# Kernel tuning notes

Hardware: AMD Instinct MI355X
Metric: run time of the kernel (lower is better)

Reference implementation:

```python
import jax, jax.numpy as jnp
import numpy as np

HIDDEN = 2048
NUM_HEADS = 16
NUM_KV_HEADS = 4
HEAD_DIM = HIDDEN // NUM_HEADS            # 128
Q_PER_KV = NUM_HEADS // NUM_KV_HEADS      # 4
GROUP_SIZE = (Q_PER_KV + 2) * HEAD_DIM    # 768
TOTAL_PROJ = NUM_KV_HEADS * GROUP_SIZE    # 3072
SEQ, BATCH = 2048, 2


def setup_inputs() -> dict:
    key = jax.random.key(0)
    k1, k2, k3 = jax.random.split(key, 3)
    x = jax.random.normal(k1, (SEQ, BATCH, HIDDEN), dtype=jnp.float32)
    weight_qkv = jax.random.normal(k2, (TOTAL_PROJ, HIDDEN), dtype=jnp.float32) * 0.02
    weight_proj = jax.random.normal(k3, (HIDDEN, NUM_HEADS * HEAD_DIM), dtype=jnp.float32) * 0.02
    return {"x": x, "weight_qkv": weight_qkv, "weight_proj": weight_proj}


def reference(x, weight_qkv, weight_proj):
    seq, batch, hidden = x.shape
    q_size = Q_PER_KV * HEAD_DIM

    # fused grouped QKV projection: [S*B, TOTAL_PROJ]
    qkv = x.reshape(-1, hidden) @ weight_qkv.T
    qkv = qkv.reshape(-1, NUM_KV_HEADS, GROUP_SIZE)
    q = qkv[:, :, :q_size].reshape(seq, batch, NUM_HEADS, HEAD_DIM)
    k = qkv[:, :, q_size:q_size + HEAD_DIM].reshape(seq, batch, NUM_KV_HEADS, HEAD_DIM)
    v = qkv[:, :, q_size + HEAD_DIM:].reshape(seq, batch, NUM_KV_HEADS, HEAD_DIM)

    # GQA: repeat_interleave kv heads to match q heads
    k = jnp.repeat(k, Q_PER_KV, axis=2)
    v = jnp.repeat(v, Q_PER_KV, axis=2)

    # [b, h, s, d]
    q = q.transpose(1, 2, 0, 3)
    k = k.transpose(1, 2, 0, 3)
    v = v.transpose(1, 2, 0, 3)

    scale = 1.0 / np.sqrt(HEAD_DIM)
    scores = jnp.einsum('bhqd,bhkd->bhqk', q, k) * scale
    causal = jnp.tril(jnp.ones((seq, seq), dtype=bool))
    scores = jnp.where(causal, scores, jnp.float32(-jnp.inf))
    probs = jax.nn.softmax(scores, axis=-1)
    attn = jnp.einsum('bhqk,bhkd->bhqd', probs, v)

    # back to [s, b, h*d] then output projection
    attn = attn.transpose(2, 0, 1, 3).reshape(seq * batch, NUM_HEADS * HEAD_DIM)
    out = attn @ weight_proj.T
    return out.reshape(seq, batch, hidden)
```

## Files before the change

### kernel.cpp

```cpp
#include <hip/hip_runtime.h>

#define SEQ 2048
#define BATCH 2
#define HIDDEN 2048
#define NHEADS 16
#define NKV 4
#define HD 128
#define GROUP 768
#define TPROJ 3072
#define NTOK (SEQ*BATCH)

typedef __attribute__((ext_vector_type(8))) __bf16 bf16x8;
typedef __attribute__((ext_vector_type(8))) unsigned short ushort8_t;
typedef __attribute__((ext_vector_type(4))) float f32x4;

union U8cast { ushort8_t u; bf16x8 b; };
__device__ inline bf16x8 as_bf(ushort8_t u) { U8cast c; c.u = u; return c.b; }

union Bf16U { __bf16 h; unsigned short u; };

__device__ inline unsigned short f2bf(float f) {
    unsigned int u = __float_as_uint(f);
    return (unsigned short)((u + 0x7FFFu + ((u >> 16) & 1u)) >> 16);
}

__device__ inline ushort8_t load8_f32_bf16(const float* __restrict__ p) {
    float4 v0 = *(const float4*)p;
    float4 v1 = *(const float4*)(p + 4);
    ushort8_t u;
    u[0] = f2bf(v0.x); u[1] = f2bf(v0.y); u[2] = f2bf(v0.z); u[3] = f2bf(v0.w);
    u[4] = f2bf(v1.x); u[5] = f2bf(v1.y); u[6] = f2bf(v1.z); u[7] = f2bf(v1.w);
    return u;
}

__device__ inline float exp2a(float x) {
    float r; asm("v_exp_f32 %0, %1" : "=v"(r) : "v"(x)); return r;
}

__device__ inline void gload_lds16(const unsigned short* g, unsigned short* l) {
    __builtin_amdgcn_global_load_lds(
        (const __attribute__((address_space(1))) void*)g,
        (__attribute__((address_space(3))) void*)l, 16, 0, 0);
}

#define CONV_N0 ((size_t)NTOK * HIDDEN)
#define CONV_N1 ((size_t)TPROJ * HIDDEN)
#define CONV_N2 ((size_t)HIDDEN * HIDDEN)
__global__ __launch_bounds__(256) void conv3_kernel(
    const float* __restrict__ x, const float* __restrict__ wq, const float* __restrict__ wp,
    unsigned short* __restrict__ xb, unsigned short* __restrict__ wqb, unsigned short* __restrict__ wpb)
{
    size_t i = (size_t)(blockIdx.x * 256 + threadIdx.x) * 8;
    if (i < CONV_N0) {
        *(ushort8_t*)(xb + i) = load8_f32_bf16(x + i);
    } else if (i < CONV_N0 + CONV_N1) {
        size_t j = i - CONV_N0;
        *(ushort8_t*)(wqb + j) = load8_f32_bf16(wq + j);
    } else {
        size_t j = i - CONV_N0 - CONV_N1;
        *(ushort8_t*)(wpb + j) = load8_f32_bf16(wp + j);
    }
}

template<bool OUT_BF16>
__global__ __launch_bounds__(512, 2) void gemm256_kernel(
    const unsigned short* __restrict__ A, const unsigned short* __restrict__ B,
    void* __restrict__ Cv, int M, int N, int K)
{
    __shared__ unsigned short lds[2][2][256 * 64];

    const int t = threadIdx.x, lane = t & 63, w = t >> 6;
    const int wm = w >> 2, wn = w & 3;
    const int l16 = lane & 15, lg = lane >> 4;

    const int cpx = (int)gridDim.x >> 3;
    const int wg  = ((int)blockIdx.x & 7) * cpx + ((int)blockIdx.x >> 3);
    const int nbn = N >> 8;
    const int m0 = (wg / nbn) << 8, n0 = (wg % nbn) << 8;
    const int NKT = K >> 6;

    const int srow = lane >> 3;
    const int scol = ((lane & 7) ^ srow) << 3;

    f32x4 acc[8][4] = {};

    auto stage = [&](const unsigned short* __restrict__ G, int g0, int kt, int op) {
        const int k0 = kt << 6;
        unsigned short* Ld = lds[kt & 1][op];
#pragma unroll
        for (int i = 0; i < 4; ++i) {
            const int r = w * 32 + i * 8;
            gload_lds16(G + (size_t)(g0 + r + srow) * K + k0 + scol, Ld + r * 64);
        }
    };

    stage(A, m0, 0, 0); stage(B, n0, 0, 1);
    stage(A, m0, 1, 0); stage(B, n0, 1, 1);

    for (int kt = 0; kt < NKT; ++kt) {
        const unsigned short* As_ = lds[kt & 1][0];
        const unsigned short* Bs_ = lds[kt & 1][1];

        if (kt < NKT - 1) asm volatile("s_waitcnt vmcnt(8)" ::: "memory");
        else              asm volatile("s_waitcnt vmcnt(0)" ::: "memory");
        __builtin_amdgcn_sched_barrier(0);
        __builtin_amdgcn_s_barrier();
        __builtin_amdgcn_sched_barrier(0);

        bf16x8 aR[8], b0R[4], b1R[4];

#pragma unroll
        for (int i = 0; i < 4; ++i)
#pragma unroll
            for (int s = 0; s < 2; ++s) {
                int row  = wm * 128 + i * 16 + l16;
                int slot = ((s << 2) | lg) ^ (l16 & 7);
                aR[i * 2 + s] = as_bf(*(const ushort8_t*)&As_[row * 64 + slot * 8]);
            }
#pragma unroll
        for (int j = 0; j < 2; ++j)
#pragma unroll
            for (int s = 0; s < 2; ++s) {
                int row  = wn * 64 + j * 16 + l16;
                int slot = ((s << 2) | lg) ^ (l16 & 7);
                b0R[j * 2 + s] = as_bf(*(const ushort8_t*)&Bs_[row * 64 + slot * 8]);
            }
        __builtin_amdgcn_s_setprio(1);
#pragma unroll
        for (int i = 0; i < 4; ++i)
#pragma unroll
            for (int j = 0; j < 2; ++j)
#pragma unroll
                for (int s = 0; s < 2; ++s)
                    acc[i][j] = __builtin_amdgcn_mfma_f32_16x16x32_bf16(aR[i*2+s], b0R[j*2+s], acc[i][j], 0, 0, 0);
        __builtin_amdgcn_s_setprio(0);

#pragma unroll
        for (int j = 0; j < 2; ++j)
#pragma unroll
            for (int s = 0; s < 2; ++s) {
                int row  = wn * 64 + 32 + j * 16 + l16;
                int slot = ((s << 2) | lg) ^ (l16 & 7);
                b1R[j * 2 + s] = as_bf(*(const ushort8_t*)&Bs_[row * 64 + slot * 8]);
            }
        __builtin_amdgcn_s_setprio(1);
#pragma unroll
        for (int i = 0; i < 4; ++i)
#pragma unroll
            for (int j = 0; j < 2; ++j)
#pragma unroll
                for (int s = 0; s < 2; ++s)
                    acc[i][2 + j] = __builtin_amdgcn_mfma_f32_16x16x32_bf16(aR[i*2+s], b1R[j*2+s], acc[i][2 + j], 0, 0, 0);
        __builtin_amdgcn_s_setprio(0);

        __builtin_amdgcn_sched_barrier(0);
        __builtin_amdgcn_s_barrier();
        __builtin_amdgcn_sched_barrier(0);
        if (kt + 2 < NKT) stage(B, n0, kt + 2, 1);
        __builtin_amdgcn_sched_barrier(0);

#pragma unroll
        for (int i = 0; i < 4; ++i)
#pragma unroll
            for (int s = 0; s < 2; ++s) {
                int row  = wm * 128 + 64 + i * 16 + l16;
                int slot = ((s << 2) | lg) ^ (l16 & 7);
                aR[i * 2 + s] = as_bf(*(const ushort8_t*)&As_[row * 64 + slot * 8]);
            }
        __builtin_amdgcn_s_setprio(1);
#pragma unroll
        for (int i = 0; i < 4; ++i)
#pragma unroll
            for (int j = 0; j < 2; ++j)
#pragma unroll
                for (int s = 0; s < 2; ++s)
                    acc[4 + i][2 + j] = __builtin_amdgcn_mfma_f32_16x16x32_bf16(aR[i*2+s], b1R[j*2+s], acc[4 + i][2 + j], 0, 0, 0);
        __builtin_amdgcn_s_setprio(0);

        __builtin_amdgcn_sched_barrier(0);
        __builtin_amdgcn_s_barrier();
        __builtin_amdgcn_sched_barrier(0);
        if (kt + 2 < NKT) stage(A, m0, kt + 2, 0);
        __builtin_amdgcn_sched_barrier(0);

        __builtin_amdgcn_s_setprio(1);
#pragma unroll
        for (int i = 0; i < 4; ++i)
#pragma unroll
            for (int j = 0; j < 2; ++j)
#pragma unroll
                for (int s = 0; s < 2; ++s)
                    acc[4 + i][j] = __builtin_amdgcn_mfma_f32_16x16x32_bf16(aR[i*2+s], b0R[j*2+s], acc[4 + i][j], 0, 0, 0);
        __builtin_amdgcn_s_setprio(0);
    }

#pragma unroll
    for (int ia = 0; ia < 8; ++ia)
#pragma unroll
        for (int jb = 0; jb < 4; ++jb)
#pragma unroll
            for (int r = 0; r < 4; ++r) {
                int row = m0 + wm * 128 + (ia >> 2) * 64 + (ia & 3) * 16 + lg * 4 + r;
                int col = n0 + wn * 64 + (jb >> 1) * 32 + (jb & 1) * 16 + l16;
                if (OUT_BF16)
                    ((unsigned short*)Cv)[(size_t)row * N + col] = f2bf(acc[ia][jb][r]);
                else
                    ((float*)Cv)[(size_t)row * N + col] = acc[ia][jb][r];
            }
}

__global__ __launch_bounds__(512, 2) void gemm_tall_kernel(
    const unsigned short* __restrict__ A, const unsigned short* __restrict__ B,
    float* __restrict__ C, int M, int N, int K)
{
    __shared__ unsigned short ldsA[2][256 * 64];
    __shared__ unsigned short ldsB[2][128 * 64];

    const int t = threadIdx.x, lane = t & 63, w = t >> 6;
    const int wm = w >> 1, wn = w & 1;
    const int l16 = lane & 15, lg = lane >> 4;

    const int cpx = (int)gridDim.x >> 3;
    const int wg  = ((int)blockIdx.x & 7) * cpx + ((int)blockIdx.x >> 3);
    const int nbn = N >> 7;
    const int m0 = (wg / nbn) << 8, n0 = (wg % nbn) << 7;
    const int NKT = K >> 6;

    const int srow = lane >> 3;
    const int scol = ((lane & 7) ^ srow) << 3;

    f32x4 acc[4][4] = {};

    auto stageA = [&](int kt) {
        const int k0 = kt << 6;
        unsigned short* Ld = ldsA[kt & 1];
#pragma unroll
        for (int i = 0; i < 4; ++i) {
            const int r = w * 32 + i * 8;
            gload_lds16(A + (size_t)(m0 + r + srow) * K + k0 + scol, Ld + r * 64);
        }
    };
    auto stageB = [&](int kt) {
        const int k0 = kt << 6;
        unsigned short* Ld = ldsB[kt & 1];
#pragma unroll
        for (int i = 0; i < 2; ++i) {
            const int r = w * 16 + i * 8;
            gload_lds16(B + (size_t)(n0 + r + srow) * K + k0 + scol, Ld + r * 64);
        }
    };

    stageA(0); stageB(0);
    stageA(1); stageB(1);

    for (int kt = 0; kt < NKT; ++kt) {
        const unsigned short* As_ = ldsA[kt & 1];
        const unsigned short* Bs_ = ldsB[kt & 1];

        if (kt < NKT - 1) asm volatile("s_waitcnt vmcnt(6)" ::: "memory");
        else              asm volatile("s_waitcnt vmcnt(0)" ::: "memory");
        __builtin_amdgcn_sched_barrier(0);
        __builtin_amdgcn_s_barrier();
        __builtin_amdgcn_sched_barrier(0);

        bf16x8 aR[4], b0R[4], b1R[4];

#pragma unroll
        for (int i = 0; i < 2; ++i)
#pragma unroll
            for (int s = 0; s < 2; ++s) {
                int row  = wm * 64 + i * 16 + l16;
                int slot = ((s << 2) | lg) ^ (l16 & 7);
                aR[i * 2 + s] = as_bf(*(const ushort8_t*)&As_[row * 64 + slot * 8]);
            }
#pragma unroll
        for (int j = 0; j < 2; ++j)
#pragma unroll
            for (int s = 0; s < 2; ++s) {
                int row  = wn * 64 + j * 16 + l16;
                int slot = ((s << 2) | lg) ^ (l16 & 7);
                b0R[j * 2 + s] = as_bf(*(const ushort8_t*)&Bs_[row * 64 + slot * 8]);
            }
        __builtin_amdgcn_s_setprio(1);
#pragma unroll
        for (int i = 0; i < 2; ++i)
#pragma unroll
            for (int j = 0; j < 2; ++j)
#pragma unroll
                for (int s = 0; s < 2; ++s)
                    acc[i][j] = __builtin_amdgcn_mfma_f32_16x16x32_bf16(aR[i*2+s], b0R[j*2+s], acc[i][j], 0, 0, 0);
        __builtin_amdgcn_s_setprio(0);

#pragma unroll
        for (int j = 0; j < 2; ++j)
#pragma unroll
            for (int s = 0; s < 2; ++s) {
                int row  = wn * 64 + 32 + j * 16 + l16;
                int slot = ((s << 2) | lg) ^ (l16 & 7);
                b1R[j * 2 + s] = as_bf(*(const ushort8_t*)&Bs_[row * 64 + slot * 8]);
            }
        __builtin_amdgcn_s_setprio(1);
#pragma unroll
        for (int i = 0; i < 2; ++i)
#pragma unroll
            for (int j = 0; j < 2; ++j)
#pragma unroll
                for (int s = 0; s < 2; ++s)
                    acc[i][2 + j] = __builtin_amdgcn_mfma_f32_16x16x32_bf16(aR[i*2+s], b1R[j*2+s], acc[i][2 + j], 0, 0, 0);
        __builtin_amdgcn_s_setprio(0);

        __builtin_amdgcn_sched_barrier(0);
        __builtin_amdgcn_s_barrier();
        __builtin_amdgcn_sched_barrier(0);
        if (kt + 2 < NKT) stageB(kt + 2);
        __builtin_amdgcn_sched_barrier(0);

#pragma unroll
        for (int i = 0; i < 2; ++i)
#pragma unroll
            for (int s = 0; s < 2; ++s) {
                int row  = wm * 64 + 32 + i * 16 + l16;
                int slot = ((s << 2) | lg) ^ (l16 & 7);
                aR[i * 2 + s] = as_bf(*(const ushort8_t*)&As_[row * 64 + slot * 8]);
            }
        __builtin_amdgcn_s_setprio(1);
#pragma unroll
        for (int i = 0; i < 2; ++i)
#pragma unroll
            for (int j = 0; j < 2; ++j)
#pragma unroll
                for (int s = 0; s < 2; ++s)
                    acc[2 + i][2 + j] = __builtin_amdgcn_mfma_f32_16x16x32_bf16(aR[i*2+s], b1R[j*2+s], acc[2 + i][2 + j], 0, 0, 0);
        __builtin_amdgcn_s_setprio(0);

        __builtin_amdgcn_sched_barrier(0);
        __builtin_amdgcn_s_barrier();
        __builtin_amdgcn_sched_barrier(0);
        if (kt + 2 < NKT) stageA(kt + 2);
        __builtin_amdgcn_sched_barrier(0);

        __builtin_amdgcn_s_setprio(1);
#pragma unroll
        for (int i = 0; i < 2; ++i)
#pragma unroll
            for (int j = 0; j < 2; ++j)
#pragma unroll
                for (int s = 0; s < 2; ++s)
                    acc[2 + i][j] = __builtin_amdgcn_mfma_f32_16x16x32_bf16(aR[i*2+s], b0R[j*2+s], acc[2 + i][j], 0, 0, 0);
        __builtin_amdgcn_s_setprio(0);
    }

#pragma unroll
    for (int i = 0; i < 4; ++i)
#pragma unroll
        for (int j = 0; j < 4; ++j)
#pragma unroll
            for (int r = 0; r < 4; ++r) {
                int row = m0 + wm * 64 + i * 16 + lg * 4 + r;
                int col = n0 + wn * 64 + j * 16 + l16;
                C[(size_t)row * N + col] = acc[i][j][r];
            }
}

__global__ __launch_bounds__(256) void vtrans_kernel(const unsigned short* __restrict__ qkv,
                                                     unsigned short* __restrict__ vT)
{
    const int t = threadIdx.x;
    const int s0 = blockIdx.x * 128 + (t & 15) * 8;
    const int bk = blockIdx.y;
    const int b_idx = bk >> 2;
    const int voff = (bk & 3) * GROUP + 640;
    const int d0 = (t >> 4) * 8;
    ushort8_t in[8];
#pragma unroll
    for (int j = 0; j < 8; ++j)
        in[j] = *(const ushort8_t*)(qkv + (size_t)((s0 + j) * BATCH + b_idx) * TPROJ + voff + d0);
#pragma unroll
    for (int dd = 0; dd < 8; ++dd) {
        ushort8_t ov;
#pragma unroll
        for (int j = 0; j < 8; ++j) ov[j] = in[j][dd];
        *(ushort8_t*)(vT + (size_t)(bk * HD + d0 + dd) * SEQ + s0) = ov;
    }
}

__global__ __launch_bounds__(256, 4) void attn_kernel(const unsigned short* __restrict__ qkv,
                                                      const unsigned short* __restrict__ vT,
                                                      unsigned short* __restrict__ attn_out)
{
    __shared__ unsigned short Ks[64][128];
    __shared__ unsigned short Vt[2][128][64];

    const int t = threadIdx.x, lane = t & 63, w = t >> 6;
    const int l16 = lane & 15, lg = lane >> 4;

    const int bid = (int)blockIdx.x;
    const int qt  = 127 - (bid >> 3);
    const int bk  = bid & 7;
    const int b_idx = bk >> 2;
    const int kvh   = bk & 3;
    const int qb0   = qt * 16;
    const int qoff  = kvh * GROUP + w * HD;
    const int koff  = kvh * GROUP + 512;
    const int vrow0 = (b_idx * NKV + kvh) * HD;
    const int h     = kvh * 4 + w;

    const float SCL2 = 0.08838834764831845f * 1.44269504f;
    const float THRU = 8.0f / SCL2;

    ushort8_t qf[4];
    {
        size_t qrow = (size_t)((qb0 + l16) * BATCH + b_idx) * TPROJ + qoff;
#pragma unroll
        for (int kc = 0; kc < 4; ++kc)
            qf[kc] = *(const ushort8_t*)(qkv + qrow + kc * 32 + lg * 8);
    }

    f32x4 o[8] = {};
    float mstate = -1e30f, lstate = 0.f, negm2 = 0.f;

    const int nIter = (qt >> 2) + 1;

    auto stageK = [&](int it) {
        const int kv0 = it << 6;
#pragma unroll
        for (int i = 0; i < 4; ++i) {
            int rl = w * 16 + i * 4 + (lane >> 4);
            int pr = 32 * ((rl >> 4) & 1) + 8 * ((rl >> 2) & 3) + 4 * (rl >> 5) + (rl & 3);
            int g  = (lane & 15) ^ (rl & 7);
            gload_lds16(qkv + (size_t)((kv0 + pr) * BATCH + b_idx) * TPROJ + koff + g * 8,
                        &Ks[w * 16 + i * 4][0]);
        }
    };
    auto stageV = [&](int it) {
        const int kv0 = it << 6;
        const int buf = it & 1;
#pragma unroll
        for (int i = 0; i < 4; ++i) {
            int rl = w * 32 + i * 8 + (lane >> 3);
            int g  = (lane & 7) ^ ((lane >> 3) & 7);
            gload_lds16(vT + (size_t)(vrow0 + rl) * SEQ + kv0 + g * 8,
                        &Vt[buf][w * 32 + i * 8][0]);
        }
    };

    stageK(0); stageV(0);

    for (int it = 0; it < nIter; ++it) {
        const int kv0 = it * 64;
        const int vbuf = it & 1;

        asm volatile("s_waitcnt vmcnt(0)" ::: "memory");
        __builtin_amdgcn_sched_barrier(0);
        __builtin_amdgcn_s_barrier();
        __builtin_amdgcn_sched_barrier(0);

        if (it + 1 < nIter) stageV(it + 1);
        __builtin_amdgcn_sched_barrier(0);

        f32x4 s[4] = {};
        __builtin_amdgcn_s_setprio(1);
#pragma unroll
        for (int nf = 0; nf < 4; ++nf)
#pragma unroll
            for (int kc = 0; kc < 4; ++kc) {
                int phys = (kc * 4 + lg) ^ (l16 & 7);
                ushort8_t kb = *(const ushort8_t*)&Ks[nf * 16 + l16][phys * 8];
                s[nf] = __builtin_amdgcn_mfma_f32_16x16x32_bf16(as_bf(kb), as_bf(qf[kc]), s[nf], 0, 0, 0);
            }
        __builtin_amdgcn_s_setprio(0);

        __builtin_amdgcn_sched_barrier(0);
        __builtin_amdgcn_s_barrier();
        __builtin_amdgcn_sched_barrier(0);
        if (it + 1 < nIter) stageK(it + 1);
        __builtin_amdgcn_sched_barrier(0);

        if (it == nIter - 1) {
            const int q_g = qb0 + l16;
#pragma unroll
            for (int nf = 0; nf < 4; ++nf)
#pragma unroll
                for (int r = 0; r < 4; ++r) {
                    int kv_g = kv0 + 32 * (nf & 1) + 8 * lg + 4 * (nf >> 1) + r;
                    if (kv_g > q_g) s[nf][r] = -1e30f;
                }
        }

        float a0 = fmaxf(fmaxf(s[0][0], s[0][1]), fmaxf(s[0][2], s[0][3]));
        float a1 = fmaxf(fmaxf(s[1][0], s[1][1]), fmaxf(s[1][2], s[1][3]));
        float a2 = fmaxf(fmaxf(s[2][0], s[2][1]), fmaxf(s[2][2], s[2][3]));
        float a3 = fmaxf(fmaxf(s[3][0], s[3][1]), fmaxf(s[3][2], s[3][3]));
        float rmax = fmaxf(fmaxf(a0, a1), fmaxf(a2, a3));
        rmax = fmaxf(rmax, __shfl_xor(rmax, 16));
        rmax = fmaxf(rmax, __shfl_xor(rmax, 32));

        if (!__all(rmax - mstate <= THRU)) {
            float mn = fmaxf(mstate, rmax);
            float corr = exp2a((mstate - mn) * SCL2);
            mstate = mn;
            negm2  = -mn * SCL2;
            lstate *= corr;
            float co[4];
#pragma unroll
            for (int r = 0; r < 4; ++r) co[r] = __shfl(corr, 4 * lg + r);
#pragma unroll
            for (int f = 0; f < 8; ++f)
#pragma unroll
                for (int r = 0; r < 4; ++r) o[f][r] *= co[r];
        }

        float rs0 = 0.f, rs1 = 0.f;
#pragma unroll
        for (int nf = 0; nf < 4; ++nf)
#pragma unroll
            for (int r = 0; r < 4; ++r) {
                float pv = exp2a(fmaf(s[nf][r], SCL2, negm2));
                s[nf][r] = pv;
                if (nf < 2) rs0 += pv; else rs1 += pv;
            }
        float rsum = rs0 + rs1;
        rsum += __shfl_xor(rsum, 16);
        rsum += __shfl_xor(rsum, 32);
        lstate += rsum;

        ushort8_t paf[2];
#pragma unroll
        for (int c = 0; c < 2; ++c)
#pragma unroll
            for (int e = 0; e < 8; ++e) {
                Bf16U cv; cv.h = (__bf16)((e < 4) ? s[c][e] : s[2 + c][e - 4]);
                paf[c][e] = cv.u;
            }

        __builtin_amdgcn_s_setprio(1);
#pragma unroll
        for (int c = 0; c < 2; ++c)
#pragma unroll
            for (int f = 0; f < 8; ++f) {
                int phys = (c * 4 + lg) ^ (l16 & 7);
                ushort8_t vf = *(const ushort8_t*)&Vt[vbuf][l16 + 16 * f][phys * 8];
                o[f] = __builtin_amdgcn_mfma_f32_16x16x32_bf16(as_bf(paf[c]), as_bf(vf), o[f], 0, 0, 0);
            }
        __builtin_amdgcn_s_setprio(0);
    }

    float li = 1.0f / lstate;
    float linv[4];
#pragma unroll
    for (int r = 0; r < 4; ++r) linv[r] = __shfl(li, 4 * lg + r);
#pragma unroll
    for (int f = 0; f < 8; ++f)
#pragma unroll
        for (int r = 0; r < 4; ++r) {
            int q_g = qb0 + lg * 4 + r;
            size_t row = (size_t)(q_g * BATCH + b_idx) * HIDDEN;
            attn_out[row + h * HD + 16 * f + l16] = f2bf(o[f][r] * linv[r]);
        }
}

extern "C" void kernel_launch(void* const* d_in, const int* in_sizes, int n_in,
                              void* d_out, int out_size, void* d_ws, size_t ws_size,
                              hipStream_t stream) {
    const float* x     = (const float*)d_in[0];
    const float* wqkv  = (const float*)d_in[1];
    const float* wproj = (const float*)d_in[2];
    float* out = (float*)d_out;

    unsigned short* qkv   = (unsigned short*)d_ws;
    unsigned short* attn  = qkv  + (size_t)NTOK * TPROJ;
    unsigned short* vT    = attn + (size_t)NTOK * HIDDEN;
    unsigned short* xb    = vT   + (size_t)BATCH * NKV * HD * SEQ;
    unsigned short* wqkvb = xb   + (size_t)NTOK * HIDDEN;
    unsigned short* wprojb= wqkvb+ (size_t)TPROJ * HIDDEN;

    conv3_kernel<<<dim3((unsigned)((CONV_N0 + CONV_N1 + CONV_N2) / 2048)), 256, 0, stream>>>(
        x, wqkv, wproj, xb, wqkvb, wprojb);

    gemm256_kernel<true><<<dim3((NTOK / 256) * (TPROJ / 256)), 512, 0, stream>>>(
        xb, wqkvb, (void*)qkv, NTOK, TPROJ, HIDDEN);

    vtrans_kernel<<<dim3(SEQ / 128, BATCH * NKV), 256, 0, stream>>>(qkv, vT);

    attn_kernel<<<dim3(1024), 256, 0, stream>>>(qkv, vT, attn);

    gemm_tall_kernel<<<dim3((NTOK / 256) * (HIDDEN / 128)), 512, 0, stream>>>(
        attn, wprojb, out, NTOK, HIDDEN, HIDDEN);
}
```

Baseline: 187.9 us.

## Process two 16-row query tiles per attention block to reuse K/V tiles

Each attention workgroup now handles 32 query rows (two 16-row sub-tiles per wave) instead of 16, so each staged K and V tile in shared memory feeds twice as many MFMAs. This halves the grid to 512 blocks and relaxes launch bounds to 2 waves per SIMD to fit the doubled accumulators and softmax state. Staging pointers are precomputed and incremented instead of recomputing addresses each iteration. The trade-off is higher register pressure, lower occupancy, and fewer blocks, which may worsen load balance across the causal triangle.

```diff
diff --git a/kernel.cpp b/kernel.cpp
--- a/kernel.cpp
+++ b/kernel.cpp
@@ -384,7 +384,7 @@
     }
 }
 
-__global__ __launch_bounds__(256, 4) void attn_kernel(const unsigned short* __restrict__ qkv,
+__global__ __launch_bounds__(256, 2) void attn_kernel(const unsigned short* __restrict__ qkv,
                                                       const unsigned short* __restrict__ vT,
                                                       unsigned short* __restrict__ attn_out)
 {
@@ -395,11 +395,11 @@
     const int l16 = lane & 15, lg = lane >> 4;
 
     const int bid = (int)blockIdx.x;
-    const int qt  = 127 - (bid >> 3);
+    const int qi  = 63 - (bid >> 3);
     const int bk  = bid & 7;
     const int b_idx = bk >> 2;
     const int kvh   = bk & 3;
-    const int qb0   = qt * 16;
+    const int qb0   = qi * 32;
     const int qoff  = kvh * GROUP + w * HD;
     const int koff  = kvh * GROUP + 512;
     const int vrow0 = (b_idx * NKV + kvh) * HD;
@@ -408,43 +408,56 @@
     const float SCL2 = 0.08838834764831845f * 1.44269504f;
     const float THRU = 8.0f / SCL2;
 
-    ushort8_t qf[4];
+    ushort8_t qf0[4], qf1[4];
     {
-        size_t qrow = (size_t)((qb0 + l16) * BATCH + b_idx) * TPROJ + qoff;
-#pragma unroll
-        for (int kc = 0; kc < 4; ++kc)
-            qf[kc] = *(const ushort8_t*)(qkv + qrow + kc * 32 + lg * 8);
-    }
-
-    f32x4 o[8] = {};
-    float mstate = -1e30f, lstate = 0.f, negm2 = 0.f;
-
-    const int nIter = (qt >> 2) + 1;
-
-    auto stageK = [&](int it) {
-        const int kv0 = it << 6;
+        size_t qrow0 = (size_t)((qb0 + l16) * BATCH + b_idx) * TPROJ + qoff;
+        size_t qrow1 = (size_t)((qb0 + 16 + l16) * BATCH + b_idx) * TPROJ + qoff;
+#pragma unroll
+        for (int kc = 0; kc < 4; ++kc) {
+            qf0[kc] = *(const ushort8_t*)(qkv + qrow0 + kc * 32 + lg * 8);
+            qf1[kc] = *(const ushort8_t*)(qkv + qrow1 + kc * 32 + lg * 8);
+        }
+    }
+
+    f32x4 o0[8] = {}, o1[8] = {};
+    float m0s = -1e30f, l0s = 0.f, n0s = 0.f;
+    float m1s = -1e30f, l1s = 0.f, n1s = 0.f;
+
+    const int nIter = (qi >> 1) + 1;
+
+    const unsigned short* kp[4];
+    const unsigned short* vp[4];
+#pragma unroll
+    for (int i = 0; i < 4; ++i) {
+        int rl = w * 16 + i * 4 + (lane >> 4);
+        int pr = 32 * ((rl >> 4) & 1) + 8 * ((rl >> 2) & 3) + 4 * (rl >> 5) + (rl & 3);
+        int g  = (lane & 15) ^ (rl & 7);
+        kp[i] = qkv + (size_t)(pr * BATCH + b_idx) * TPROJ + koff + g * 8;
+    }
+#pragma unroll
+    for (int i = 0; i < 4; ++i) {
+        int rl = w * 32 + i * 8 + (lane >> 3);
+        int g  = (lane & 7) ^ ((lane >> 3) & 7);
+        vp[i] = vT + (size_t)(vrow0 + rl) * SEQ + g * 8;
+    }
+    const size_t KSTR = (size_t)64 * BATCH * TPROJ;
+
+    auto stageK = [&]() {
 #pragma unroll
         for (int i = 0; i < 4; ++i) {
-            int rl = w * 16 + i * 4 + (lane >> 4);
-            int pr = 32 * ((rl >> 4) & 1) + 8 * ((rl >> 2) & 3) + 4 * (rl >> 5) + (rl & 3);
-            int g  = (lane & 15) ^ (rl & 7);
-            gload_lds16(qkv + (size_t)((kv0 + pr) * BATCH + b_idx) * TPROJ + koff + g * 8,
-                        &Ks[w * 16 + i * 4][0]);
+            gload_lds16(kp[i], &Ks[w * 16 + i * 4][0]);
+            kp[i] += KSTR;
         }
     };
-    auto stageV = [&](int it) {
-        const int kv0 = it << 6;
-        const int buf = it & 1;
+    auto stageV = [&](int buf) {
 #pragma unroll
         for (int i = 0; i < 4; ++i) {
-            int rl = w * 32 + i * 8 + (lane >> 3);
-            int g  = (lane & 7) ^ ((lane >> 3) & 7);
-            gload_lds16(vT + (size_t)(vrow0 + rl) * SEQ + kv0 + g * 8,
-                        &Vt[buf][w * 32 + i * 8][0]);
+            gload_lds16(vp[i], &Vt[buf][w * 32 + i * 8][0]);
+            vp[i] += 64;
         }
     };
 
-    stageK(0); stageV(0);
+    stageK(); stageV(0);
 
     for (int it = 0; it < nIter; ++it) {
         const int kv0 = it * 64;
@@ -455,10 +468,10 @@
         __builtin_amdgcn_s_barrier();
         __builtin_amdgcn_sched_barrier(0);
 
-        if (it + 1 < nIter) stageV(it + 1);
-        __builtin_amdgcn_sched_barrier(0);
-
-        f32x4 s[4] = {};
+        if (it + 1 < nIter) stageV(vbuf ^ 1);
+        __builtin_amdgcn_sched_barrier(0);
+
+        f32x4 s0[4] = {}, s1[4] = {};
         __builtin_amdgcn_s_setprio(1);
 #pragma unroll
         for (int nf = 0; nf < 4; ++nf)
@@ -466,71 +479,101 @@
             for (int kc = 0; kc < 4; ++kc) {
                 int phys = (kc * 4 + lg) ^ (l16 & 7);
                 ushort8_t kb = *(const ushort8_t*)&Ks[nf * 16 + l16][phys * 8];
-                s[nf] = __builtin_amdgcn_mfma_f32_16x16x32_bf16(as_bf(kb), as_bf(qf[kc]), s[nf], 0, 0, 0);
-            }
-        __builtin_amdgcn_s_setprio(0);
-
-        __builtin_amdgcn_sched_barrier(0);
-        __builtin_amdgcn_s_barrier();
-        __builtin_amdgcn_sched_barrier(0);
-        if (it + 1 < nIter) stageK(it + 1);
+                s0[nf] = __builtin_amdgcn_mfma_f32_16x16x32_bf16(as_bf(kb), as_bf(qf0[kc]), s0[nf], 0, 0, 0);
+                s1[nf] = __builtin_amdgcn_mfma_f32_16x16x32_bf16(as_bf(kb), as_bf(qf1[kc]), s1[nf], 0, 0, 0);
+            }
+        __builtin_amdgcn_s_setprio(0);
+
+        __builtin_amdgcn_sched_barrier(0);
+        __builtin_amdgcn_s_barrier();
+        __builtin_amdgcn_sched_barrier(0);
+        if (it + 1 < nIter) stageK();
         __builtin_amdgcn_sched_barrier(0);
 
         if (it == nIter - 1) {
-            const int q_g = qb0 + l16;
+            const int qg0 = qb0 + l16;
+            const int qg1 = qb0 + 16 + l16;
 #pragma unroll
             for (int nf = 0; nf < 4; ++nf)
 #pragma unroll
                 for (int r = 0; r < 4; ++r) {
                     int kv_g = kv0 + 32 * (nf & 1) + 8 * lg + 4 * (nf >> 1) + r;
-                    if (kv_g > q_g) s[nf][r] = -1e30f;
+                    if (kv_g > qg0) s0[nf][r] = -1e30f;
+                    if (kv_g > qg1) s1[nf][r] = -1e30f;
                 }
         }
 
-        float a0 = fmaxf(fmaxf(s[0][0], s[0][1]), fmaxf(s[0][2], s[0][3]));
-        float a1 = fmaxf(fmaxf(s[1][0], s[1][1]), fmaxf(s[1][2], s[1][3]));
-        float a2 = fmaxf(fmaxf(s[2][0], s[2][1]), fmaxf(s[2][2], s[2][3]));
-        float a3 = fmaxf(fmaxf(s[3][0], s[3][1]), fmaxf(s[3][2], s[3][3]));
-        float rmax = fmaxf(fmaxf(a0, a1), fmaxf(a2, a3));
-        rmax = fmaxf(rmax, __shfl_xor(rmax, 16));
-        rmax = fmaxf(rmax, __shfl_xor(rmax, 32));
-
-        if (!__all(rmax - mstate <= THRU)) {
-            float mn = fmaxf(mstate, rmax);
-            float corr = exp2a((mstate - mn) * SCL2);
-            mstate = mn;
-            negm2  = -mn * SCL2;
-            lstate *= corr;
-            float co[4];
-#pragma unroll
-            for (int r = 0; r < 4; ++r) co[r] = __shfl(corr, 4 * lg + r);
-#pragma unroll
-            for (int f = 0; f < 8; ++f)
-#pragma unroll
-                for (int r = 0; r < 4; ++r) o[f][r] *= co[r];
-        }
-
-        float rs0 = 0.f, rs1 = 0.f;
+        float rmax0, rmax1;
+        {
+            float a0 = fmaxf(fmaxf(s0[0][0], s0[0][1]), fmaxf(s0[0][2], s0[0][3]));
+            float a1 = fmaxf(fmaxf(s0[1][0], s0[1][1]), fmaxf(s0[1][2], s0[1][3]));
+            float a2 = fmaxf(fmaxf(s0[2][0], s0[2][1]), fmaxf(s0[2][2], s0[2][3]));
+            float a3 = fmaxf(fmaxf(s0[3][0], s0[3][1]), fmaxf(s0[3][2], s0[3][3]));
+            rmax0 = fmaxf(fmaxf(a0, a1), fmaxf(a2, a3));
+            float b0 = fmaxf(fmaxf(s1[0][0], s1[0][1]), fmaxf(s1[0][2], s1[0][3]));
+            float b1 = fmaxf(fmaxf(s1[1][0], s1[1][1]), fmaxf(s1[1][2], s1[1][3]));
+            float b2 = fmaxf(fmaxf(s1[2][0], s1[2][1]), fmaxf(s1[2][2], s1[2][3]));
+            float b3 = fmaxf(fmaxf(s1[3][0], s1[3][1]), fmaxf(s1[3][2], s1[3][3]));
+            rmax1 = fmaxf(fmaxf(b0, b1), fmaxf(b2, b3));
+        }
+        rmax0 = fmaxf(rmax0, __shfl_xor(rmax0, 16));
+        rmax0 = fmaxf(rmax0, __shfl_xor(rmax0, 32));
+        rmax1 = fmaxf(rmax1, __shfl_xor(rmax1, 16));
+        rmax1 = fmaxf(rmax1, __shfl_xor(rmax1, 32));
+
+        float gmx = fmaxf(rmax0 - m0s, rmax1 - m1s);
+        if (!__all(gmx <= THRU)) {
+            {
+                float mn = fmaxf(m0s, rmax0);
+                float corr = exp2a((m0s - mn) * SCL2);
+                m0s = mn; n0s = -mn * SCL2; l0s *= corr;
+                float co[4];
+#pragma unroll
+                for (int r = 0; r < 4; ++r) co[r] = __shfl(corr, 4 * lg + r);
+#pragma unroll
+                for (int f = 0; f < 8; ++f)
+#pragma unroll
+                    for (int r = 0; r < 4; ++r) o0[f][r] *= co[r];
+            }
+            {
+                float mn = fmaxf(m1s, rmax1);
+                float corr = exp2a((m1s - mn) * SCL2);
+                m1s = mn; n1s = -mn * SCL2; l1s *= corr;
+                float co[4];
+#pragma unroll
+                for (int r = 0; r < 4; ++r) co[r] = __shfl(corr, 4 * lg + r);
+#pragma unroll
+                for (int f = 0; f < 8; ++f)
+#pragma unroll
+                    for (int r = 0; r < 4; ++r) o1[f][r] *= co[r];
+            }
+        }
+
+        float rsum0 = 0.f, rsum1 = 0.f;
 #pragma unroll
         for (int nf = 0; nf < 4; ++nf)
 #pragma unroll
             for (int r = 0; r < 4; ++r) {
-                float pv = exp2a(fmaf(s[nf][r], SCL2, negm2));
-                s[nf][r] = pv;
-                if (nf < 2) rs0 += pv; else rs1 += pv;
-            }
-        float rsum = rs0 + rs1;
-        rsum += __shfl_xor(rsum, 16);
-        rsum += __shfl_xor(rsum, 32);
-        lstate += rsum;
-
-        ushort8_t paf[2];
+                float p0 = exp2a(fmaf(s0[nf][r], SCL2, n0s));
+                float p1 = exp2a(fmaf(s1[nf][r], SCL2, n1s));
+                s0[nf][r] = p0; s1[nf][r] = p1;
+                rsum0 += p0; rsum1 += p1;
+            }
+        rsum0 += __shfl_xor(rsum0, 16);
+        rsum0 += __shfl_xor(rsum0, 32);
+        rsum1 += __shfl_xor(rsum1, 16);
+        rsum1 += __shfl_xor(rsum1, 32);
+        l0s += rsum0; l1s += rsum1;
+
+        ushort8_t paf0[2], paf1[2];
 #pragma unroll
         for (int c = 0; c < 2; ++c)
 #pragma unroll
             for (int e = 0; e < 8; ++e) {
-                Bf16U cv; cv.h = (__bf16)((e < 4) ? s[c][e] : s[2 + c][e - 4]);
-                paf[c][e] = cv.u;
+                Bf16U c0; c0.h = (__bf16)((e < 4) ? s0[c][e] : s0[2 + c][e - 4]);
+                paf0[c][e] = c0.u;
+                Bf16U c1; c1.h = (__bf16)((e < 4) ? s1[c][e] : s1[2 + c][e - 4]);
+                paf1[c][e] = c1.u;
             }
 
         __builtin_amdgcn_s_setprio(1);
@@ -540,22 +583,27 @@
             for (int f = 0; f < 8; ++f) {
                 int phys = (c * 4 + lg) ^ (l16 & 7);
                 ushort8_t vf = *(const ushort8_t*)&Vt[vbuf][l16 + 16 * f][phys * 8];
-                o[f] = __builtin_amdgcn_mfma_f32_16x16x32_bf16(as_bf(paf[c]), as_bf(vf), o[f], 0, 0, 0);
-            }
-        __builtin_amdgcn_s_setprio(0);
-    }
-
-    float li = 1.0f / lstate;
-    float linv[4];
-#pragma unroll
-    for (int r = 0; r < 4; ++r) linv[r] = __shfl(li, 4 * lg + r);
+                o0[f] = __builtin_amdgcn_mfma_f32_16x16x32_bf16(as_bf(paf0[c]), as_bf(vf), o0[f], 0, 0, 0);
+                o1[f] = __builtin_amdgcn_mfma_f32_16x16x32_bf16(as_bf(paf1[c]), as_bf(vf), o1[f], 0, 0, 0);
+            }
+        __builtin_amdgcn_s_setprio(0);
+    }
+
+    float li0 = 1.0f / l0s, li1 = 1.0f / l1s;
+    float lv0[4], lv1[4];
+#pragma unroll
+    for (int r = 0; r < 4; ++r) {
+        lv0[r] = __shfl(li0, 4 * lg + r);
+        lv1[r] = __shfl(li1, 4 * lg + r);
+    }
 #pragma unroll
     for (int f = 0; f < 8; ++f)
 #pragma unroll
         for (int r = 0; r < 4; ++r) {
-            int q_g = qb0 + lg * 4 + r;
-            size_t row = (size_t)(q_g * BATCH + b_idx) * HIDDEN;
-            attn_out[row + h * HD + 16 * f + l16] = f2bf(o[f][r] * linv[r]);
+            int q0 = qb0 + lg * 4 + r;
+            int q1 = qb0 + 16 + lg * 4 + r;
+            attn_out[(size_t)(q0 * BATCH + b_idx) * HIDDEN + h * HD + 16 * f + l16] = f2bf(o0[f][r] * lv0[r]);
+            attn_out[(size_t)(q1 * BATCH + b_idx) * HIDDEN + h * HD + 16 * f + l16] = f2bf(o1[f][r] * lv1[r]);
         }
 }
 
@@ -582,7 +630,7 @@
 
     vtrans_kernel<<<dim3(SEQ / 128, BATCH * NKV), 256, 0, stream>>>(qkv, vT);
 
-    attn_kernel<<<dim3(1024), 256, 0, stream>>>(qkv, vT, attn);
+    attn_kernel<<<dim3(512), 256, 0, stream>>>(qkv, vT, attn);
 
     gemm_tall_kernel<<<dim3((NTOK / 256) * (HIDDEN / 128)), 512, 0, stream>>>(
         attn, wprojb, out, NTOK, HIDDEN, HIDDEN);
```

Measured after the change: 193.1 us. 2.8% more time.

## Split GEMM tile loads into quarter-tile stages interleaved with MFMA phases

Applied to the files above, without the earlier changes.

Restructures the 256x256 GEMM main loop so global-to-LDS loads are issued in four half-operand chunks, each interleaved with one of the four MFMA sub-phases. Each phase is bracketed by workgroup barriers and lgkmcnt waits, in a ping-pong style schedule. The aim is to spread memory traffic evenly across the iteration and overlap it with matrix math, with one iteration of lookahead for B and two for A. The cost is more barriers per k-step and a more fragile vmcnt accounting scheme.

```diff
diff --git a/kernel.cpp b/kernel.cpp
--- a/kernel.cpp
+++ b/kernel.cpp
@@ -84,114 +84,143 @@
 
     f32x4 acc[8][4] = {};
 
-    auto stage = [&](const unsigned short* __restrict__ G, int g0, int kt, int op) {
+    auto stA = [&](int kt, int e) {
         const int k0 = kt << 6;
-        unsigned short* Ld = lds[kt & 1][op];
-#pragma unroll
-        for (int i = 0; i < 4; ++i) {
-            const int r = w * 32 + i * 8;
-            gload_lds16(G + (size_t)(g0 + r + srow) * K + k0 + scol, Ld + r * 64);
+        unsigned short* Ld = lds[kt & 1][0];
+#pragma unroll
+        for (int hh = 0; hh < 2; ++hh) {
+            int r = (e + 2 * hh) * 64 + w * 8;
+            gload_lds16(A + (size_t)(m0 + r + srow) * K + k0 + scol, Ld + r * 64);
         }
     };
-
-    stage(A, m0, 0, 0); stage(B, n0, 0, 1);
-    stage(A, m0, 1, 0); stage(B, n0, 1, 1);
+    auto stB = [&](int kt, int e) {
+        const int k0 = kt << 6;
+        unsigned short* Ld = lds[kt & 1][1];
+#pragma unroll
+        for (int hh = 0; hh < 2; ++hh) {
+            int r = (e * 2 + hh) * 64 + w * 8;
+            gload_lds16(B + (size_t)(n0 + r + srow) * K + k0 + scol, Ld + r * 64);
+        }
+    };
+
+    stA(0, 0); stA(0, 1); stB(0, 0); stB(0, 1);
+    if (NKT > 1) { stA(1, 0); stB(1, 0); stA(1, 1); }
+    if (NKT > 1) asm volatile("s_waitcnt vmcnt(6)" ::: "memory");
+    else         asm volatile("s_waitcnt vmcnt(0)" ::: "memory");
+    __builtin_amdgcn_sched_barrier(0);
+    __builtin_amdgcn_s_barrier();
+    __builtin_amdgcn_sched_barrier(0);
 
     for (int kt = 0; kt < NKT; ++kt) {
         const unsigned short* As_ = lds[kt & 1][0];
         const unsigned short* Bs_ = lds[kt & 1][1];
 
-        if (kt < NKT - 1) asm volatile("s_waitcnt vmcnt(8)" ::: "memory");
+        bf16x8 aR[8], b0R[4], b1R[4];
+
+#pragma unroll
+        for (int i = 0; i < 4; ++i)
+#pragma unroll
+            for (int s = 0; s < 2; ++s) {
+                int row  = wm * 128 + i * 16 + l16;
+                int slot = ((s << 2) | lg) ^ (l16 & 7);
+                aR[i * 2 + s] = as_bf(*(const ushort8_t*)&As_[row * 64 + slot * 8]);
+            }
+#pragma unroll
+        for (int j = 0; j < 2; ++j)
+#pragma unroll
+            for (int s = 0; s < 2; ++s) {
+                int row  = wn * 64 + j * 16 + l16;
+                int slot = ((s << 2) | lg) ^ (l16 & 7);
+                b0R[j * 2 + s] = as_bf(*(const ushort8_t*)&Bs_[row * 64 + slot * 8]);
+            }
+        if (kt + 1 < NKT) stB(kt + 1, 1);
+        __builtin_amdgcn_sched_barrier(0);
+        __builtin_amdgcn_s_barrier();
+        asm volatile("s_waitcnt lgkmcnt(0)" ::: "memory");
+        __builtin_amdgcn_sched_barrier(0);
+        __builtin_amdgcn_s_setprio(1);
+#pragma unroll
+        for (int i = 0; i < 4; ++i)
+#pragma unroll
+            for (int j = 0; j < 2; ++j)
+#pragma unroll
+                for (int s = 0; s < 2; ++s)
+                    acc[i][j] = __builtin_amdgcn_mfma_f32_16x16x32_bf16(aR[i*2+s], b0R[j*2+s], acc[i][j], 0, 0, 0);
+        __builtin_amdgcn_s_setprio(0);
+        __builtin_amdgcn_sched_barrier(0);
+        __builtin_amdgcn_s_barrier();
+        __builtin_amdgcn_sched_barrier(0);
+
+#pragma unroll
+        for (int j = 0; j < 2; ++j)
+#pragma unroll
+            for (int s = 0; s < 2; ++s) {
+                int row  = wn * 64 + 32 + j * 16 + l16;
+                int slot = ((s << 2) | lg) ^ (l16 & 7);
+                b1R[j * 2 + s] = as_bf(*(const ushort8_t*)&Bs_[row * 64 + slot * 8]);
+            }
+        if (kt + 2 < NKT) stA(kt + 2, 0);
+        __builtin_amdgcn_sched_barrier(0);
+        __builtin_amdgcn_s_barrier();
+        asm volatile("s_waitcnt lgkmcnt(0)" ::: "memory");
+        __builtin_amdgcn_sched_barrier(0);
+        __builtin_amdgcn_s_setprio(1);
+#pragma unroll
+        for (int i = 0; i < 4; ++i)
+#pragma unroll
+            for (int j = 0; j < 2; ++j)
+#pragma unroll
+                for (int s = 0; s < 2; ++s)
+                    acc[i][2 + j] = __builtin_amdgcn_mfma_f32_16x16x32_bf16(aR[i*2+s], b1R[j*2+s], acc[i][2 + j], 0, 0, 0);
+        __builtin_amdgcn_s_setprio(0);
+        __builtin_amdgcn_sched_barrier(0);
+        __builtin_amdgcn_s_barrier();
+        __builtin_amdgcn_sched_barrier(0);
+
+#pragma unroll
+        for (int i = 0; i < 4; ++i)
+#pragma unroll
+            for (int s = 0; s < 2; ++s) {
+                int row  = wm * 128 + 64 + i * 16 + l16;
+                int slot = ((s << 2) | lg) ^ (l16 & 7);
+                aR[i * 2 + s] = as_bf(*(const ushort8_t*)&As_[row * 64 + slot * 8]);
+            }
+        if (kt + 2 < NKT) stB(kt + 2, 0);
+        __builtin_amdgcn_sched_barrier(0);
+        __builtin_amdgcn_s_barrier();
+        asm volatile("s_waitcnt lgkmcnt(0)" ::: "memory");
+        __builtin_amdgcn_sched_barrier(0);
+        __builtin_amdgcn_s_setprio(1);
+#pragma unroll
+        for (int i = 0; i < 4; ++i)
+#pragma unroll
+            for (int j = 0; j < 2; ++j)
+#pragma unroll
+                for (int s = 0; s < 2; ++s)
+                    acc[4 + i][2 + j] = __builtin_amdgcn_mfma_f32_16x16x32_bf16(aR[i*2+s], b1R[j*2+s], acc[4 + i][2 + j], 0, 0, 0);
+        __builtin_amdgcn_s_setprio(0);
+        __builtin_amdgcn_sched_barrier(0);
+        __builtin_amdgcn_s_barrier();
+        __builtin_amdgcn_sched_barrier(0);
+
+        if (kt + 2 < NKT) stA(kt + 2, 1);
+        if (kt + 2 < NKT) asm volatile("s_waitcnt vmcnt(6)" ::: "memory");
         else              asm volatile("s_waitcnt vmcnt(0)" ::: "memory");
         __builtin_amdgcn_sched_barrier(0);
         __builtin_amdgcn_s_barrier();
         __builtin_amdgcn_sched_barrier(0);
-
-        bf16x8 aR[8], b0R[4], b1R[4];
-
+        __builtin_amdgcn_s_setprio(1);
 #pragma unroll
         for (int i = 0; i < 4; ++i)
 #pragma unroll
-            for (int s = 0; s < 2; ++s) {
-                int row  = wm * 128 + i * 16 + l16;
-                int slot = ((s << 2) | lg) ^ (l16 & 7);
-                aR[i * 2 + s] = as_bf(*(const ushort8_t*)&As_[row * 64 + slot * 8]);
-            }
-#pragma unroll
-        for (int j = 0; j < 2; ++j)
-#pragma unroll
-            for (int s = 0; s < 2; ++s) {
-                int row  = wn * 64 + j * 16 + l16;
-                int slot = ((s << 2) | lg) ^ (l16 & 7);
-                b0R[j * 2 + s] = as_bf(*(const ushort8_t*)&Bs_[row * 64 + slot * 8]);
-            }
-        __builtin_amdgcn_s_setprio(1);
-#pragma unroll
-        for (int i = 0; i < 4; ++i)
-#pragma unroll
-            for (int j = 0; j < 2; ++j)
-#pragma unroll
-                for (int s = 0; s < 2; ++s)
-                    acc[i][j] = __builtin_amdgcn_mfma_f32_16x16x32_bf16(aR[i*2+s], b0R[j*2+s], acc[i][j], 0, 0, 0);
-        __builtin_amdgcn_s_setprio(0);
-
-#pragma unroll
-        for (int j = 0; j < 2; ++j)
-#pragma unroll
-            for (int s = 0; s < 2; ++s) {
-                int row  = wn * 64 + 32 + j * 16 + l16;
-                int slot = ((s << 2) | lg) ^ (l16 & 7);
-                b1R[j * 2 + s] = as_bf(*(const ushort8_t*)&Bs_[row * 64 + slot * 8]);
-            }
-        __builtin_amdgcn_s_setprio(1);
-#pragma unroll
-        for (int i = 0; i < 4; ++i)
-#pragma unroll
-            for (int j = 0; j < 2; ++j)
-#pragma unroll
-                for (int s = 0; s < 2; ++s)
-                    acc[i][2 + j] = __builtin_amdgcn_mfma_f32_16x16x32_bf16(aR[i*2+s], b1R[j*2+s], acc[i][2 + j], 0, 0, 0);
-        __builtin_amdgcn_s_setprio(0);
-
-        __builtin_amdgcn_sched_barrier(0);
-        __builtin_amdgcn_s_barrier();
-        __builtin_amdgcn_sched_barrier(0);
-        if (kt + 2 < NKT) stage(B, n0, kt + 2, 1);
-        __builtin_amdgcn_sched_barrier(0);
-
-#pragma unroll
-        for (int i = 0; i < 4; ++i)
-#pragma unroll
-            for (int s = 0; s < 2; ++s) {
-                int row  = wm * 128 + 64 + i * 16 + l16;
-                int slot = ((s << 2) | lg) ^ (l16 & 7);
-                aR[i * 2 + s] = as_bf(*(const ushort8_t*)&As_[row * 64 + slot * 8]);
-            }
-        __builtin_amdgcn_s_setprio(1);
-#pragma unroll
-        for (int i = 0; i < 4; ++i)
-#pragma unroll
-            for (int j = 0; j < 2; ++j)
-#pragma unroll
-                for (int s = 0; s < 2; ++s)
-                    acc[4 + i][2 + j] = __builtin_amdgcn_mfma_f32_16x16x32_bf16(aR[i*2+s], b1R[j*2+s], acc[4 + i][2 + j], 0, 0, 0);
-        __builtin_amdgcn_s_setprio(0);
-
-        __builtin_amdgcn_sched_barrier(0);
-        __builtin_amdgcn_s_barrier();
-        __builtin_amdgcn_sched_barrier(0);
-        if (kt + 2 < NKT) stage(A, m0, kt + 2, 0);
-        __builtin_amdgcn_sched_barrier(0);
-
-        __builtin_amdgcn_s_setprio(1);
-#pragma unroll
-        for (int i = 0; i < 4; ++i)
-#pragma unroll
             for (int j = 0; j < 2; ++j)
 #pragma unroll
                 for (int s = 0; s < 2; ++s)
                     acc[4 + i][j] = __builtin_amdgcn_mfma_f32_16x16x32_bf16(aR[i*2+s], b0R[j*2+s], acc[4 + i][j], 0, 0, 0);
         __builtin_amdgcn_s_setprio(0);
+        __builtin_amdgcn_sched_barrier(0);
+        __builtin_amdgcn_s_barrier();
+        __builtin_amdgcn_sched_barrier(0);
     }
 
 #pragma unroll
```

Result: no change. 190.3 us (+1.3%).
